# Kernel tuning notes

Measured on AMD Instinct MI355X. Metric: run time of the kernel, lower is better.

Reference implementation:

```python
import jax, jax.numpy as jnp
import numpy as np

N, E, F_IN, H, EF, G, GFD = 50000, 800000, 64, 128, 8, 10, 2
NEG_SLOPE = 0.2  # PyG GATv2Conv default negative_slope


def _gatv2_layer(x, src, dst, edge_attr, Wl, bl, Wr, br, We, att, bias):
    # PyG GATv2Conv, heads=1, concat=True, share_weights=False
    n = x.shape[0]
    xl = x @ Wl + bl            # source transform [N,H]
    xr = x @ Wr + br            # target transform [N,H]
    e = edge_attr @ We          # edge embedding   [E,H]
    s = jax.nn.leaky_relu(xl[src] + xr[dst] + e, NEG_SLOPE)  # [E,H]
    logits = s @ att            # [E]
    # numerically-stable segment softmax over destination nodes
    mx = jax.ops.segment_max(logits, dst, num_segments=n)
    mx = jnp.where(jnp.isfinite(mx), mx, 0.0)
    ex = jnp.exp(logits - mx[dst])
    den = jax.ops.segment_sum(ex, dst, num_segments=n)
    alpha = ex / jnp.maximum(den[dst], 1e-16)
    out = jax.ops.segment_sum(alpha[:, None] * xl[src], dst, num_segments=n)
    return out + bias


def _forward(x, edge_index, edge_attr, graph_features, num_graphs, params, head_W, head_b):
    src, dst = edge_index[0], edge_index[1]
    for (Wl, bl, Wr, br, We, att, bias) in params:
        x = jax.nn.relu(_gatv2_layer(x, src, dst, edge_attr, Wl, bl, Wr, br, We, att, bias))
        # dropout p=0.0 / eval mode: no-op
    n_nodes = x.shape[0] // num_graphs
    # faithful replication of the torch reshape chain (graph_feature_dim == 2):
    # graph_features.T [GFD,G] -> unsqueeze(2) -> repeat to [GFD,G,Np] -> view(G,GFD,Np)
    # -> cat(unbind(0), dim=1) -> [GFD, G*Np]
    gf = jnp.broadcast_to(graph_features.T[:, :, None], (GFD, num_graphs, n_nodes))
    gf = gf.reshape(num_graphs, GFD, n_nodes)
    gf = gf.transpose(1, 0, 2).reshape(GFD, num_graphs * n_nodes)
    x = jnp.concatenate([x, gf.T], axis=1)  # [N, H+GFD]
    return x @ head_W + head_b


def setup_inputs():
    key = jax.random.key(0)
    ks = list(jax.random.split(key, 32))
    p = lambda k, s: jax.random.normal(k, s, jnp.float32) * 0.05
    inp = {
        'x': jax.random.normal(ks[0], (N, F_IN), jnp.float32),
        'edge_index': jax.random.randint(ks[1], (2, E), 0, N),
        'edge_attr': jax.random.normal(ks[2], (E, EF), jnp.float32),
        'graph_features': jax.random.normal(ks[3], (G, GFD), jnp.float32),
        'num_graphs': G,
    }
    i = 4
    for l in range(3):
        fin = F_IN if l == 0 else H
        inp[f'Wl{l}'] = p(ks[i], (fin, H)); i += 1
        inp[f'bl{l}'] = jnp.zeros((H,), jnp.float32)
        inp[f'Wr{l}'] = p(ks[i], (fin, H)); i += 1
        inp[f'br{l}'] = jnp.zeros((H,), jnp.float32)
        inp[f'We{l}'] = p(ks[i], (EF, H)); i += 1
        inp[f'att{l}'] = p(ks[i], (H,)); i += 1
        inp[f'bias{l}'] = jnp.zeros((H,), jnp.float32)
    inp['head_W'] = p(ks[i], (H + GFD, 1))
    inp['head_b'] = jnp.zeros((1,), jnp.float32)
    return inp


def reference(x, edge_index, edge_attr, graph_features, num_graphs,
              Wl0, bl0, Wr0, br0, We0, att0, bias0,
              Wl1, bl1, Wr1, br1, We1, att1, bias1,
              Wl2, bl2, Wr2, br2, We2, att2, bias2,
              head_W, head_b):
    params = [(Wl0, bl0, Wr0, br0, We0, att0, bias0),
              (Wl1, bl1, Wr1, br1, We1, att1, bias1),
              (Wl2, bl2, Wr2, br2, We2, att2, bias2)]
    return _forward(x, edge_index, edge_attr, graph_features, num_graphs, params, head_W, head_b)
```

## Files before the change

kernel.cpp:

```cpp
#include <hip/hip_runtime.h>
#include <hip/hip_bf16.h>
#include <math.h>

#define NN 50000
#define EE 800000
#define F_IN 64
#define HH 128
#define EF 8
#define GG 10
#define GFD 2
#define NEG_SLOPE 0.2f
#define NB 64

__device__ __forceinline__ void fma4(float4& a, float s, const float4& b) {
  a.x = fmaf(s, b.x, a.x); a.y = fmaf(s, b.y, a.y);
  a.z = fmaf(s, b.z, a.z); a.w = fmaf(s, b.w, a.w);
}
__device__ __forceinline__ float lrelu1(float x) {
  return fmaf(NEG_SLOPE, fminf(x, 0.f), fmaxf(x, 0.f));
}

template <int CTRL>
__device__ __forceinline__ float dpp_add(float v) {
  int p = __builtin_amdgcn_update_dpp(0, __float_as_int(v), CTRL, 0xf, 0xf, true);
  return v + __int_as_float(p);
}
__device__ __forceinline__ float red32(float v) {
  v = dpp_add<0xB1>(v);
  v = dpp_add<0x4E>(v);
  v = dpp_add<0x141>(v);
  v = dpp_add<0x140>(v);
  v += __int_as_float(__builtin_amdgcn_ds_swizzle(__float_as_int(v), 0x401F));
  return v;
}

__global__ __launch_bounds__(256) void lin2_kernel(
    const float* __restrict__ x, int fin,
    const float* __restrict__ Wl, const float* __restrict__ bl,
    const float* __restrict__ Wr, const float* __restrict__ br,
    float* __restrict__ xl, float* __restrict__ xr, int n_nodes) {
  __shared__ float xs[64 * 128];
  const int tid = threadIdx.x;
  const int base = blockIdx.x * 64;
  int nrows = n_nodes - base; if (nrows > 64) nrows = 64;

  const int total4 = (nrows * fin) >> 2;
  const float4* xsrc = (const float4*)(x + (size_t)base * fin);
  float4* xd = (float4*)xs;
  for (int i = tid; i < total4; i += 256) xd[i] = xsrc[i];
  __syncthreads();

  const int lane = tid & 63;
  const int w = tid >> 6;
  const int c = lane * 2;

  float accl0[16], accl1[16], accr0[16], accr1[16];
#pragma unroll
  for (int j = 0; j < 16; j++) { accl0[j]=0.f; accl1[j]=0.f; accr0[j]=0.f; accr1[j]=0.f; }

  const float* xrow = xs + (w * 16) * fin;
  for (int k = 0; k < fin; k += 2) {
    float2 wl0 = *(const float2*)(Wl + (size_t)k * HH + c);
    float2 wl1 = *(const float2*)(Wl + (size_t)(k + 1) * HH + c);
    float2 wr0 = *(const float2*)(Wr + (size_t)k * HH + c);
    float2 wr1 = *(const float2*)(Wr + (size_t)(k + 1) * HH + c);
#pragma unroll
    for (int j = 0; j < 16; j++) {
      float2 xv = *(const float2*)(xrow + j * fin + k);
      accl0[j] = fmaf(xv.x, wl0.x, accl0[j]);
      accl1[j] = fmaf(xv.x, wl0.y, accl1[j]);
      accr0[j] = fmaf(xv.x, wr0.x, accr0[j]);
      accr1[j] = fmaf(xv.x, wr0.y, accr1[j]);
      accl0[j] = fmaf(xv.y, wl1.x, accl0[j]);
      accl1[j] = fmaf(xv.y, wl1.y, accl1[j]);
      accr0[j] = fmaf(xv.y, wr1.x, accr0[j]);
      accr1[j] = fmaf(xv.y, wr1.y, accr1[j]);
    }
  }
  float2 blv = *(const float2*)(bl + c);
  float2 brv = *(const float2*)(br + c);
#pragma unroll
  for (int j = 0; j < 16; j++) {
    int n = base + w * 16 + j;
    if (n < n_nodes) {
      *(float2*)(xl + (size_t)n * HH + c) = make_float2(accl0[j] + blv.x, accl1[j] + blv.y);
      *(float2*)(xr + (size_t)n * HH + c) = make_float2(accr0[j] + brv.x, accr1[j] + brv.y);
    }
  }
}

__global__ __launch_bounds__(256) void hist_kernel(const int* __restrict__ dst,
                                                   int* __restrict__ hist, int ne) {
  int i = blockIdx.x * blockDim.x + threadIdx.x;
  if (i < ne) atomicAdd(&hist[dst[i]], 1);
}

__global__ __launch_bounds__(1024) void reduce_kernel(const int* __restrict__ hist,
                                                      int* __restrict__ bsum, int n) {
  __shared__ int wsum[16];
  const int tid = threadIdx.x;
  const int lane = tid & 63, w = tid >> 6;
  int i = blockIdx.x * 1024 + tid;
  int v = (i < n) ? hist[i] : 0;
#pragma unroll
  for (int off = 32; off; off >>= 1) v += __shfl_xor(v, off);
  if (lane == 0) wsum[w] = v;
  __syncthreads();
  if (tid < 16) {
    int s = wsum[tid];
#pragma unroll
    for (int off = 8; off; off >>= 1) s += __shfl_xor(s, off);
    if (tid == 0) bsum[blockIdx.x] = s;
  }
}

__global__ __launch_bounds__(64) void scanb_kernel(const int* __restrict__ bsum,
                                                   int* __restrict__ bbase,
                                                   int* __restrict__ offs, int nb, int n) {
  const int tid = threadIdx.x;
  int v = (tid < nb) ? bsum[tid] : 0;
  int inc = v;
#pragma unroll
  for (int d = 1; d < 64; d <<= 1) {
    int t2 = __shfl_up(inc, d);
    if (tid >= d) inc += t2;
  }
  if (tid < nb) bbase[tid] = inc - v;
  if (tid == 63) offs[n] = inc;
}

__global__ __launch_bounds__(1024) void scanc_kernel(const int* __restrict__ hist,
                                                     const int* __restrict__ bbase,
                                                     int* __restrict__ offs,
                                                     int* __restrict__ cursor, int n) {
  __shared__ int wsum[16], wpre[16];
  const int tid = threadIdx.x;
  const int lane = tid & 63, w = tid >> 6;
  int i = blockIdx.x * 1024 + tid;
  int orig = (i < n) ? hist[i] : 0;
  int v = orig;
#pragma unroll
  for (int d = 1; d < 64; d <<= 1) {
    int t2 = __shfl_up(v, d);
    if (lane >= d) v += t2;
  }
  if (lane == 63) wsum[w] = v;
  __syncthreads();
  if (tid < 16) {
    int s = wsum[tid];
    int inc = s;
#pragma unroll
    for (int d = 1; d < 16; d <<= 1) {
      int t2 = __shfl_up(inc, d);
      if (tid >= d) inc += t2;
    }
    wpre[tid] = inc - s;
  }
  __syncthreads();
  if (i < n) {
    int ex = bbase[blockIdx.x] + wpre[w] + (v - orig);
    offs[i] = ex; cursor[i] = ex;
  }
}

__global__ __launch_bounds__(256) void scatter_kernel(
    const int* __restrict__ src, const int* __restrict__ dst,
    int* __restrict__ cursor, int2* __restrict__ pk, int ne) {
  int i = blockIdx.x * blockDim.x + threadIdx.x;
  if (i < ne) {
    int d = dst[i];
    int pos = atomicAdd(&cursor[d], 1);
    pk[pos] = make_int2(src[i] * 512, i * 32);
  }
}

__global__ __launch_bounds__(256) void deg_hist_kernel(const int* __restrict__ offs,
                                                       int* __restrict__ hist2, int n) {
  __shared__ int lhist[NB];
  const int tid = threadIdx.x;
  int i = blockIdx.x * 256 + tid;
  if (tid < NB) lhist[tid] = 0;
  __syncthreads();
  if (i < n) {
    int d = offs[i + 1] - offs[i];
    int key = NB - 1 - min(d, NB - 1);
    atomicAdd(&lhist[key], 1);
  }
  __syncthreads();
  if (tid < NB && lhist[tid]) atomicAdd(&hist2[tid], lhist[tid]);
}

__global__ __launch_bounds__(64) void scan64_kernel(const int* __restrict__ hist2,
                                                    int* __restrict__ cursor2) {
  const int tid = threadIdx.x;
  int v = hist2[tid];
  int inc = v;
#pragma unroll
  for (int d = 1; d < 64; d <<= 1) {
    int t2 = __shfl_up(inc, d);
    if (tid >= d) inc += t2;
  }
  cursor2[tid] = inc - v;
}

__global__ __launch_bounds__(256) void deg_scatter_kernel(const int* __restrict__ offs,
                                                          int* __restrict__ cursor2,
                                                          int* __restrict__ nperm, int n) {
  __shared__ int lhist[NB];
  __shared__ int lbase[NB];
  const int tid = threadIdx.x;
  int i = blockIdx.x * 256 + tid;
  if (tid < NB) lhist[tid] = 0;
  __syncthreads();
  int key = 0, rank = 0;
  const bool valid = (i < n);
  if (valid) {
    int d = offs[i + 1] - offs[i];
    key = NB - 1 - min(d, NB - 1);
    rank = atomicAdd(&lhist[key], 1);
  }
  __syncthreads();
  if (tid < NB && lhist[tid]) lbase[tid] = atomicAdd(&cursor2[tid], lhist[tid]);
  __syncthreads();
  if (valid) nperm[lbase[key] + rank] = i;
}

__global__ __launch_bounds__(256, 4) void gat_fused_kernel(
    const float* __restrict__ xl, const float* __restrict__ xr,
    const float* __restrict__ ea, const float* __restrict__ We,
    const float* __restrict__ att,
    const int2* __restrict__ pk, const int* __restrict__ offs,
    const int* __restrict__ nperm, const float* __restrict__ bias,
    float* __restrict__ xout, int n_nodes) {
  const int lane = threadIdx.x & 63;
  const int g = lane >> 5, t = lane & 31;
  const int c = t * 4;
  const int tb = t * 16;
  const int nwaves = gridDim.x * 4;

  float4 we[EF];
#pragma unroll
  for (int k = 0; k < EF; k++) we[k] = *(const float4*)(We + k * HH + c);
  const float4 at = *(const float4*)(att + c);
  const float4 bi = *(const float4*)(bias + c);
  const char* xlb = (const char*)xl;
  const char* eab = (const char*)ea;

  for (int wid = blockIdx.x * 4 + (threadIdx.x >> 6); wid < n_nodes; wid += nwaves) {
    const int node = nperm[wid];
    const int b = offs[node], e = offs[node + 1];
    const int deg = e - b;

    if (deg == 0) {
      if (g == 0) {
        float4 o;
        o.x = fmaxf(bi.x, 0.f); o.y = fmaxf(bi.y, 0.f);
        o.z = fmaxf(bi.z, 0.f); o.w = fmaxf(bi.w, 0.f);
        *(float4*)(xout + (size_t)node * HH + c) = o;
      }
      continue;
    }

    const float4 vr = *(const float4*)(xr + (size_t)node * HH + c);
    const int emax = e - 1;

    float4 acc = make_float4(0.f, 0.f, 0.f, 0.f);
    float den = 0.f;
    float4 vlA, eaPA, eaQA, vlB, eaPB, eaQB;

#define LOADS(VL, EP, EQ, IDX)                                      \
  do {                                                              \
    int _cx = min((IDX), emax);                                     \
    int2 _o = pk[_cx];                                              \
    VL = *(const float4*)(xlb + (_o.x + tb));                       \
    EP = *(const float4*)(eab + _o.y);                              \
    EQ = *(const float4*)(eab + (_o.y + 16));                       \
  } while (0)

#define PROCESS(VL, EP, EQ, IDX)                                     \
  do {                                                               \
    float4 s = make_float4(VL.x + vr.x, VL.y + vr.y, VL.z + vr.z,    \
                           VL.w + vr.w);                             \
    fma4(s, EP.x, we[0]); fma4(s, EP.y, we[1]);                      \
    fma4(s, EP.z, we[2]); fma4(s, EP.w, we[3]);                      \
    fma4(s, EQ.x, we[4]); fma4(s, EQ.y, we[5]);                      \
    fma4(s, EQ.z, we[6]); fma4(s, EQ.w, we[7]);                      \
    float v = lrelu1(s.x) * at.x;                                    \
    v = fmaf(lrelu1(s.y), at.y, v);                                  \
    v = fmaf(lrelu1(s.z), at.z, v);                                  \
    v = fmaf(lrelu1(s.w), at.w, v);                                  \
    v = red32(v);                                                    \
    const float p = ((IDX) < e) ? __expf(v) : 0.f;                   \
    den += p;                                                        \
    fma4(acc, p, VL);                                                \
  } while (0)

    int idx = b + g;
    LOADS(vlA, eaPA, eaQA, idx);
    LOADS(vlB, eaPB, eaQB, idx + 2);

    const int nit = (deg + 3) >> 2;
    for (int j = 0; j < nit; j++) {
      PROCESS(vlA, eaPA, eaQA, idx);
      LOADS(vlA, eaPA, eaQA, idx + 4);
      PROCESS(vlB, eaPB, eaQB, idx + 2);
      LOADS(vlB, eaPB, eaQB, idx + 6);
      idx += 4;
    }
#undef LOADS
#undef PROCESS

    den += __shfl_xor(den, 32);
    acc.x += __shfl_xor(acc.x, 32);
    acc.y += __shfl_xor(acc.y, 32);
    acc.z += __shfl_xor(acc.z, 32);
    acc.w += __shfl_xor(acc.w, 32);

    if (g == 0) {
      const float inv = 1.f / fmaxf(den, 1e-16f);
      float4 o;
      o.x = fmaxf(fmaf(acc.x, inv, bi.x), 0.f);
      o.y = fmaxf(fmaf(acc.y, inv, bi.y), 0.f);
      o.z = fmaxf(fmaf(acc.z, inv, bi.z), 0.f);
      o.w = fmaxf(fmaf(acc.w, inv, bi.w), 0.f);
      *(float4*)(xout + (size_t)node * HH + c) = o;
    }
  }
}

__global__ __launch_bounds__(256) void head_kernel(
    const float* __restrict__ x, const float* __restrict__ gf,
    const float* __restrict__ hw, const float* __restrict__ hb,
    float* __restrict__ out, int n_nodes) {
  const int lane = threadIdx.x & 63;
  const int nwaves = gridDim.x * 4;
  const float w0 = hw[lane], w1 = hw[lane + 64];
  for (int wid = blockIdx.x * 4 + (threadIdx.x >> 6); wid < n_nodes; wid += nwaves) {
    const float* xp = x + (size_t)wid * HH;
    float v = xp[lane] * w0 + xp[lane + 64] * w1;
#pragma unroll
    for (int off = 32; off; off >>= 1) v += __shfl_xor(v, off);
    if (lane == 0) {
      int k = wid / (NN / GG);
      int i0 = 2 * k, i1 = 2 * k + 1;
      float g0 = gf[(i0 % GG) * GFD + (i0 / GG)];
      float g1 = gf[(i1 % GG) * GFD + (i1 / GG)];
      v += g0 * hw[HH] + g1 * hw[HH + 1] + hb[0];
      out[wid] = v;
    }
  }
}

extern "C" void kernel_launch(void* const* d_in, const int* in_sizes, int n_in,
                              void* d_out, int out_size, void* d_ws, size_t ws_size,
                              hipStream_t stream) {
  const float* x_in = (const float*)d_in[0];
  const int*   eidx = (const int*)d_in[1];
  const float* ea   = (const float*)d_in[2];
  const float* gf   = (const float*)d_in[3];
  const int* src = eidx;
  const int* dst = eidx + EE;
  const float* head_W = (const float*)d_in[26];
  const float* head_b = (const float*)d_in[27];
  float* out = (float*)d_out;

  const int NCHUNK = (NN + 1023) / 1024;

  float* P      = (float*)d_ws;
  float* Q      = P + (size_t)NN * HH;
  float* R      = Q + (size_t)NN * HH;
  int2*  pk     = (int2*)(R + (size_t)NN * HH);
  int*   hist   = (int*)(pk + EE);
  int*   offs   = hist + NN;
  int*   cursor = offs + NN + 1;
  int*   hist2  = cursor + NN;
  int*   cursor2= hist2 + NB;
  int*   nperm  = cursor2 + NB;
  int*   bsum   = nperm + NN;
  int*   bbase  = bsum + NCHUNK;

  (void)hipMemsetAsync(hist, 0, NN * sizeof(int), stream);
  (void)hipMemsetAsync(hist2, 0, NB * sizeof(int), stream);
  hist_kernel<<<(EE + 255) / 256, 256, 0, stream>>>(dst, hist, EE);
  reduce_kernel<<<NCHUNK, 1024, 0, stream>>>(hist, bsum, NN);
  scanb_kernel<<<1, 64, 0, stream>>>(bsum, bbase, offs, NCHUNK, NN);
  scanc_kernel<<<NCHUNK, 1024, 0, stream>>>(hist, bbase, offs, cursor, NN);
  scatter_kernel<<<(EE + 255) / 256, 256, 0, stream>>>(src, dst, cursor, pk, EE);
  deg_hist_kernel<<<(NN + 255) / 256, 256, 0, stream>>>(offs, hist2, NN);
  scan64_kernel<<<1, 64, 0, stream>>>(hist2, cursor2);
  deg_scatter_kernel<<<(NN + 255) / 256, 256, 0, stream>>>(offs, cursor2, nperm, NN);

  const float* xcur = x_in;
  int fin = F_IN;
  for (int l = 0; l < 3; l++) {
    const float* Wl   = (const float*)d_in[5 + 7 * l + 0];
    const float* bl   = (const float*)d_in[5 + 7 * l + 1];
    const float* Wr   = (const float*)d_in[5 + 7 * l + 2];
    const float* br   = (const float*)d_in[5 + 7 * l + 3];
    const float* We   = (const float*)d_in[5 + 7 * l + 4];
    const float* att  = (const float*)d_in[5 + 7 * l + 5];
    const float* bias = (const float*)d_in[5 + 7 * l + 6];

    lin2_kernel<<<(NN + 63) / 64, 256, 0, stream>>>(xcur, fin, Wl, bl, Wr, br, P, Q, NN);
    gat_fused_kernel<<<2048, 256, 0, stream>>>(P, Q, ea, We, att, pk,
                                               offs, nperm, bias, R, NN);
    xcur = R;
    fin = HH;
  }
  head_kernel<<<2048, 256, 0, stream>>>(R, gf, head_W, head_b, out, NN);
}
```

Before: 550.4 us.

## Store edge attributes in CSR order and fuse the output head into the last layer

The scatter pass now also copies each edge's 8 attributes into a destination-sorted array. The aggregation kernel can then read them contiguously by CSR position instead of gathering by original edge id, and the packed index shrinks to just the source offset. The final linear head is folded into the third GAT layer, which saves writing and re-reading the last hidden features, and leaky-relu becomes a single max. The cost is an extra permuted copy of edge_attr in workspace and a heavier scatter pass. The graph-feature pointer is passed through the xout argument and some dead code is left behind.

```diff
diff --git a/kernel.cpp b/kernel.cpp
--- a/kernel.cpp
+++ b/kernel.cpp
@@ -17,7 +17,7 @@
   a.z = fmaf(s, b.z, a.z); a.w = fmaf(s, b.w, a.w);
 }
 __device__ __forceinline__ float lrelu1(float x) {
-  return fmaf(NEG_SLOPE, fminf(x, 0.f), fmaxf(x, 0.f));
+  return fmaxf(x, NEG_SLOPE * x);
 }
 
 template <int CTRL>
@@ -165,12 +165,15 @@
 
 __global__ __launch_bounds__(256) void scatter_kernel(
     const int* __restrict__ src, const int* __restrict__ dst,
-    int* __restrict__ cursor, int2* __restrict__ pk, int ne) {
+    int* __restrict__ cursor, int* __restrict__ pk,
+    const float4* __restrict__ ea4, float4* __restrict__ eas, int ne) {
   int i = blockIdx.x * blockDim.x + threadIdx.x;
   if (i < ne) {
     int d = dst[i];
     int pos = atomicAdd(&cursor[d], 1);
-    pk[pos] = make_int2(src[i] * 512, i * 32);
+    pk[pos] = src[i] * 512;
+    float4 a = ea4[i * 2], b = ea4[i * 2 + 1];
+    eas[pos * 2] = a; eas[pos * 2 + 1] = b;
   }
 }
 
@@ -227,11 +230,13 @@
 
 __global__ __launch_bounds__(256, 4) void gat_fused_kernel(
     const float* __restrict__ xl, const float* __restrict__ xr,
-    const float* __restrict__ ea, const float* __restrict__ We,
+    const float* __restrict__ eas, const float* __restrict__ We,
     const float* __restrict__ att,
-    const int2* __restrict__ pk, const int* __restrict__ offs,
+    const int* __restrict__ pk, const int* __restrict__ offs,
     const int* __restrict__ nperm, const float* __restrict__ bias,
-    float* __restrict__ xout, int n_nodes) {
+    float* __restrict__ xout, int n_nodes,
+    float* __restrict__ out_head, const float* __restrict__ hw,
+    const float* __restrict__ hb) {
   const int lane = threadIdx.x & 63;
   const int g = lane >> 5, t = lane & 31;
   const int c = t * 4;
@@ -244,37 +249,38 @@
   const float4 at = *(const float4*)(att + c);
   const float4 bi = *(const float4*)(bias + c);
   const char* xlb = (const char*)xl;
-  const char* eab = (const char*)ea;
+  const char* easb = (const char*)eas;
+  float4 hwv = make_float4(0.f, 0.f, 0.f, 0.f);
+  float hw0 = 0.f, hw1 = 0.f, hb0 = 0.f;
+  if (out_head) {
+    hwv = *(const float4*)(hw + c);
+    hw0 = hw[HH]; hw1 = hw[HH + 1]; hb0 = hb[0];
+  }
 
   for (int wid = blockIdx.x * 4 + (threadIdx.x >> 6); wid < n_nodes; wid += nwaves) {
     const int node = nperm[wid];
     const int b = offs[node], e = offs[node + 1];
     const int deg = e - b;
 
+    float4 o;
     if (deg == 0) {
-      if (g == 0) {
-        float4 o;
-        o.x = fmaxf(bi.x, 0.f); o.y = fmaxf(bi.y, 0.f);
-        o.z = fmaxf(bi.z, 0.f); o.w = fmaxf(bi.w, 0.f);
-        *(float4*)(xout + (size_t)node * HH + c) = o;
-      }
-      continue;
-    }
-
-    const float4 vr = *(const float4*)(xr + (size_t)node * HH + c);
-    const int emax = e - 1;
-
-    float4 acc = make_float4(0.f, 0.f, 0.f, 0.f);
-    float den = 0.f;
-    float4 vlA, eaPA, eaQA, vlB, eaPB, eaQB;
+      o.x = fmaxf(bi.x, 0.f); o.y = fmaxf(bi.y, 0.f);
+      o.z = fmaxf(bi.z, 0.f); o.w = fmaxf(bi.w, 0.f);
+    } else {
+      const float4 vr = *(const float4*)(xr + (size_t)node * HH + c);
+      const int emax = e - 1;
+
+      float4 acc = make_float4(0.f, 0.f, 0.f, 0.f);
+      float den = 0.f;
+      float4 vlA, eaPA, eaQA, vlB, eaPB, eaQB;
 
 #define LOADS(VL, EP, EQ, IDX)                                      \
   do {                                                              \
     int _cx = min((IDX), emax);                                     \
-    int2 _o = pk[_cx];                                              \
-    VL = *(const float4*)(xlb + (_o.x + tb));                       \
-    EP = *(const float4*)(eab + _o.y);                              \
-    EQ = *(const float4*)(eab + (_o.y + 16));                       \
+    EP = *(const float4*)(easb + (_cx << 5));                       \
+    EQ = *(const float4*)(easb + (_cx << 5) + 16);                  \
+    int _ob = pk[_cx];                                              \
+    VL = *(const float4*)(xlb + (_ob + tb));                        \
   } while (0)
 
 #define PROCESS(VL, EP, EQ, IDX)                                     \
@@ -295,58 +301,49 @@
     fma4(acc, p, VL);                                                \
   } while (0)
 
-    int idx = b + g;
-    LOADS(vlA, eaPA, eaQA, idx);
-    LOADS(vlB, eaPB, eaQB, idx + 2);
-
-    const int nit = (deg + 3) >> 2;
-    for (int j = 0; j < nit; j++) {
-      PROCESS(vlA, eaPA, eaQA, idx);
-      LOADS(vlA, eaPA, eaQA, idx + 4);
-      PROCESS(vlB, eaPB, eaQB, idx + 2);
-      LOADS(vlB, eaPB, eaQB, idx + 6);
-      idx += 4;
-    }
+      int idx = b + g;
+      LOADS(vlA, eaPA, eaQA, idx);
+      LOADS(vlB, eaPB, eaQB, idx + 2);
+
+      const int nit = (deg + 3) >> 2;
+      for (int j = 0; j < nit; j++) {
+        PROCESS(vlA, eaPA, eaQA, idx);
+        LOADS(vlA, eaPA, eaQA, idx + 4);
+        PROCESS(vlB, eaPB, eaQB, idx + 2);
+        LOADS(vlB, eaPB, eaQB, idx + 6);
+        idx += 4;
+      }
 #undef LOADS
 #undef PROCESS
 
-    den += __shfl_xor(den, 32);
-    acc.x += __shfl_xor(acc.x, 32);
-    acc.y += __shfl_xor(acc.y, 32);
-    acc.z += __shfl_xor(acc.z, 32);
-    acc.w += __shfl_xor(acc.w, 32);
-
-    if (g == 0) {
+      den += __shfl_xor(den, 32);
+      acc.x += __shfl_xor(acc.x, 32);
+      acc.y += __shfl_xor(acc.y, 32);
+      acc.z += __shfl_xor(acc.z, 32);
+      acc.w += __shfl_xor(acc.w, 32);
+
       const float inv = 1.f / fmaxf(den, 1e-16f);
-      float4 o;
       o.x = fmaxf(fmaf(acc.x, inv, bi.x), 0.f);
       o.y = fmaxf(fmaf(acc.y, inv, bi.y), 0.f);
       o.z = fmaxf(fmaf(acc.z, inv, bi.z), 0.f);
       o.w = fmaxf(fmaf(acc.w, inv, bi.w), 0.f);
-      *(float4*)(xout + (size_t)node * HH + c) = o;
-    }
-  }
-}
-
-__global__ __launch_bounds__(256) void head_kernel(
-    const float* __restrict__ x, const float* __restrict__ gf,
-    const float* __restrict__ hw, const float* __restrict__ hb,
-    float* __restrict__ out, int n_nodes) {
-  const int lane = threadIdx.x & 63;
-  const int nwaves = gridDim.x * 4;
-  const float w0 = hw[lane], w1 = hw[lane + 64];
-  for (int wid = blockIdx.x * 4 + (threadIdx.x >> 6); wid < n_nodes; wid += nwaves) {
-    const float* xp = x + (size_t)wid * HH;
-    float v = xp[lane] * w0 + xp[lane + 64] * w1;
-#pragma unroll
-    for (int off = 32; off; off >>= 1) v += __shfl_xor(v, off);
-    if (lane == 0) {
-      int k = wid / (NN / GG);
-      int i0 = 2 * k, i1 = 2 * k + 1;
-      float g0 = gf[(i0 % GG) * GFD + (i0 / GG)];
-      float g1 = gf[(i1 % GG) * GFD + (i1 / GG)];
-      v += g0 * hw[HH] + g1 * hw[HH + 1] + hb[0];
-      out[wid] = v;
+    }
+
+    if (!out_head) {
+      if (g == 0) *(float4*)(xout + (size_t)node * HH + c) = o;
+    } else {
+      float hv = o.x * hwv.x + o.y * hwv.y + o.z * hwv.z + o.w * hwv.w;
+      hv = red32(hv);
+      if (lane == 0) {
+        int k = node / (NN / GG);
+        int i0 = 2 * k, i1 = 2 * k + 1;
+        float g0 = hw0 * ((const float*)out_head == nullptr ? 0.f : 1.f);
+        g0 = __ldg(&((const float*)hb)[0]);
+        (void)g0;
+        float gf0 = xout[(i0 % GG) * GFD + (i0 / GG)];
+        float gf1 = xout[(i1 % GG) * GFD + (i1 / GG)];
+        out_head[node] = hv + gf0 * hw0 + gf1 * hw1 + hb0;
+      }
     }
   }
 }
@@ -369,8 +366,9 @@
   float* P      = (float*)d_ws;
   float* Q      = P + (size_t)NN * HH;
   float* R      = Q + (size_t)NN * HH;
-  int2*  pk     = (int2*)(R + (size_t)NN * HH);
-  int*   hist   = (int*)(pk + EE);
+  float* eas    = R + (size_t)NN * HH;
+  int*   pk     = (int*)(eas + (size_t)EE * EF);
+  int*   hist   = pk + EE;
   int*   offs   = hist + NN;
   int*   cursor = offs + NN + 1;
   int*   hist2  = cursor + NN;
@@ -385,7 +383,8 @@
   reduce_kernel<<<NCHUNK, 1024, 0, stream>>>(hist, bsum, NN);
   scanb_kernel<<<1, 64, 0, stream>>>(bsum, bbase, offs, NCHUNK, NN);
   scanc_kernel<<<NCHUNK, 1024, 0, stream>>>(hist, bbase, offs, cursor, NN);
-  scatter_kernel<<<(EE + 255) / 256, 256, 0, stream>>>(src, dst, cursor, pk, EE);
+  scatter_kernel<<<(EE + 255) / 256, 256, 0, stream>>>(src, dst, cursor, pk,
+                                                       (const float4*)ea, (float4*)eas, EE);
   deg_hist_kernel<<<(NN + 255) / 256, 256, 0, stream>>>(offs, hist2, NN);
   scan64_kernel<<<1, 64, 0, stream>>>(hist2, cursor2);
   deg_scatter_kernel<<<(NN + 255) / 256, 256, 0, stream>>>(offs, cursor2, nperm, NN);
@@ -402,10 +401,14 @@
     const float* bias = (const float*)d_in[5 + 7 * l + 6];
 
     lin2_kernel<<<(NN + 63) / 64, 256, 0, stream>>>(xcur, fin, Wl, bl, Wr, br, P, Q, NN);
-    gat_fused_kernel<<<2048, 256, 0, stream>>>(P, Q, ea, We, att, pk,
-                                               offs, nperm, bias, R, NN);
+    if (l < 2) {
+      gat_fused_kernel<<<2048, 256, 0, stream>>>(P, Q, eas, We, att, pk, offs, nperm,
+                                                 bias, R, NN, nullptr, nullptr, nullptr);
+    } else {
+      gat_fused_kernel<<<2048, 256, 0, stream>>>(P, Q, eas, We, att, pk, offs, nperm,
+                                                 bias, (float*)gf, NN, out, head_W, head_b);
+    }
     xcur = R;
     fin = HH;
   }
-  head_kernel<<<2048, 256, 0, stream>>>(R, gf, head_W, head_b, out, NN);
-}
+}
```

After: 506.3 us. -8.0%, faster.
